# Kernel optimization log

Hardware: AMD Instinct MI355X
Metric: run time of the kernel (lower is better)

## Reference

```python
import jax, jax.numpy as jnp
import numpy as np

N = 8192
D_IN = 256
D_OUT = 256


def setup_inputs() -> dict:
    key = jax.random.key(0)
    k1, k2, k3 = jax.random.split(key, 3)
    input = jax.random.normal(k1, (N, D_IN), dtype=jnp.float32)
    adjacencyMatrix = jax.random.uniform(k2, (N, N), dtype=jnp.float32)
    W = jax.random.normal(k3, (D_OUT, D_IN), dtype=jnp.float32) * (1.0 / np.sqrt(D_IN))
    return {"input": input, "adjacencyMatrix": adjacencyMatrix, "W": W}


def reference(input, adjacencyMatrix, W):
    # degree^{-1/2} from row sums
    d_inv_sqrt = jnp.sum(adjacencyMatrix, axis=1) ** -0.5  # [N]
    # D^{-1/2} A D^{-1/2} as row/column scaling (same math as diag matmuls)
    A_norm = adjacencyMatrix * d_inv_sqrt[:, None] * d_inv_sqrt[None, :]  # [N, N]
    # A_norm @ X @ W^T (nn.Linear without bias)
    h = A_norm @ input            # [N, D_IN]
    return h @ W.T                # [N, D_OUT]
```

## Files before the change

### kernel.cpp

```cpp
#include <hip/hip_runtime.h>
#include <stdint.h>

#define NROWS 8192
#define KDIM  8192
#define DIN   256
#define DOUT  256

typedef __attribute__((ext_vector_type(8))) short bf16x8;
typedef __attribute__((ext_vector_type(4))) float f32x4;

__device__ __forceinline__ unsigned short f2bf(float f) {
    union { float f; unsigned u; } v; v.f = f;
    unsigned r = v.u + 0x7FFFu + ((v.u >> 16) & 1u);
    return (unsigned short)(r >> 16);
}

__device__ __forceinline__ void async_load16(const void* g, void* l) {
    __builtin_amdgcn_global_load_lds(
        (__attribute__((address_space(1))) void*)(void*)g,
        (__attribute__((address_space(3))) void*)l, 16, 0, 0);
}

__global__ __launch_bounds__(256) void k_rowsum(const float* __restrict__ A,
                                                float* __restrict__ dis) {
    const int wave = threadIdx.x >> 6, lane = threadIdx.x & 63;
    const int row = (blockIdx.x << 2) + wave;
    const float4* rp = (const float4*)(A + (size_t)row * KDIM);
    float s0 = 0.f, s1 = 0.f, s2 = 0.f, s3 = 0.f;
    #pragma unroll
    for (int it = 0; it < 32; it += 4) {
        float4 v0 = rp[(it + 0) * 64 + lane];
        float4 v1 = rp[(it + 1) * 64 + lane];
        float4 v2 = rp[(it + 2) * 64 + lane];
        float4 v3 = rp[(it + 3) * 64 + lane];
        s0 += (v0.x + v0.y) + (v0.z + v0.w);
        s1 += (v1.x + v1.y) + (v1.z + v1.w);
        s2 += (v2.x + v2.y) + (v2.z + v2.w);
        s3 += (v3.x + v3.y) + (v3.z + v3.w);
    }
    float s = (s0 + s1) + (s2 + s3);
    #pragma unroll
    for (int off = 32; off > 0; off >>= 1) s += __shfl_down(s, off, 64);
    if (lane == 0) dis[row] = rsqrtf(s);
}

__global__ __launch_bounds__(256, 2) void k_xw(const float* __restrict__ X,
                                               const float* __restrict__ W,
                                               const float* __restrict__ dis,
                                               unsigned short* __restrict__ Zst) {
    __shared__ short sX[64 * 72];
    __shared__ short sW[256 * 72];
    __shared__ float disS[64];
    const int tid = threadIdx.x;
    const int w = tid >> 6, lane = tid & 63, lm = lane & 15, lq = lane >> 4;
    const int j0 = blockIdx.x * 64;
    if (tid < 64) disS[tid] = dis[j0 + tid];
    f32x4 acc[4][4] = {};

    for (int s = 0; s < 4; ++s) {
        const int k0 = s * 64;
        #pragma unroll
        for (int i = 0; i < 4; ++i) {
            int e = tid + i * 256;
            int row = e >> 4, c4 = e & 15;
            float4 v = *(const float4*)(X + (size_t)(j0 + row) * DIN + k0 + c4 * 4);
            short4 b; b.x = (short)f2bf(v.x); b.y = (short)f2bf(v.y);
            b.z = (short)f2bf(v.z); b.w = (short)f2bf(v.w);
            *(short4*)&sX[row * 72 + c4 * 4] = b;
        }
        #pragma unroll
        for (int i = 0; i < 16; ++i) {
            int e = tid + i * 256;
            int row = e >> 4, c4 = e & 15;
            float4 v = *(const float4*)(W + (size_t)row * DIN + k0 + c4 * 4);
            short4 b; b.x = (short)f2bf(v.x); b.y = (short)f2bf(v.y);
            b.z = (short)f2bf(v.z); b.w = (short)f2bf(v.w);
            *(short4*)&sW[row * 72 + c4 * 4] = b;
        }
        __syncthreads();
        #pragma unroll
        for (int kk = 0; kk < 2; ++kk) {
            const int koff = kk * 32 + lq * 8;
            bf16x8 a[4], b[4];
            #pragma unroll
            for (int mt = 0; mt < 4; ++mt)
                a[mt] = *(const bf16x8*)&sX[(mt * 16 + lm) * 72 + koff];
            #pragma unroll
            for (int nt = 0; nt < 4; ++nt)
                b[nt] = *(const bf16x8*)&sW[(w * 64 + nt * 16 + lm) * 72 + koff];
            #pragma unroll
            for (int mt = 0; mt < 4; ++mt)
                #pragma unroll
                for (int nt = 0; nt < 4; ++nt)
                    acc[mt][nt] = __builtin_amdgcn_mfma_f32_16x16x32_bf16(
                        a[mt], b[nt], acc[mt][nt], 0, 0, 0);
        }
        __syncthreads();
    }

    #pragma unroll
    for (int mt = 0; mt < 4; ++mt)
        #pragma unroll
        for (int nt = 0; nt < 4; ++nt)
            #pragma unroll
            for (int r = 0; r < 4; ++r) {
                int jl = mt * 16 + lq * 4 + r;
                int n  = w * 64 + nt * 16 + lm;
                float v = acc[mt][nt][r] * disS[jl];
                sW[n * 72 + jl] = (short)f2bf(v);
            }
    __syncthreads();
    #pragma unroll
    for (int it = 0; it < 8; ++it) {
        int e = tid + it * 256;
        int n = e >> 3, ch = e & 7;
        bf16x8 val = *(const bf16x8*)&sW[n * 72 + ch * 8];
        *(bf16x8*)(Zst + (size_t)n * NROWS + j0 + ch * 8) = val;
    }
}

template <bool ATOMIC>
__global__ __launch_bounds__(512, 2) void k_gemm2(const float* __restrict__ A,
                                                  const unsigned short* __restrict__ Zst,
                                                  const float* __restrict__ dis,
                                                  float* __restrict__ out) {
    __shared__ short sA[2][128 * 72];
    __shared__ short sB[2][256 * 64];
    __shared__ float disS[128];
    const int tid = threadIdx.x;
    const int w = tid >> 6, lane = tid & 63, lm = lane & 15, lq = lane >> 4;
    const int wm = w >> 2, wn = w & 3;
    const int m0 = blockIdx.x * 128;
    const int split = blockIdx.y;
    const int kbase = split * 2048;
    if (tid < 128) disS[tid] = dis[m0 + tid];
    f32x4 acc[4][4] = {};
    const int swz_c = (lane & 7) ^ (lane >> 3);
    const int arow = tid >> 4, ac = tid & 15;
    float4 va[4];

#define LOAD_A(K0)                                                                   \
    do {                                                                             \
        _Pragma("unroll")                                                            \
        for (int i = 0; i < 4; ++i)                                                  \
            va[i] = *(const float4*)(A + (size_t)(m0 + arow + i * 32) * KDIM + (K0) + ac * 4); \
    } while (0)

#define WRITE_A(BUF)                                                                 \
    do {                                                                             \
        _Pragma("unroll")                                                            \
        for (int i = 0; i < 4; ++i) {                                                \
            short4 b; b.x = (short)f2bf(va[i].x); b.y = (short)f2bf(va[i].y);        \
            b.z = (short)f2bf(va[i].z); b.w = (short)f2bf(va[i].w);                  \
            *(short4*)&sA[BUF][(arow + i * 32) * 72 + ac * 4] = b;                   \
        }                                                                            \
    } while (0)

#define STAGE_B(BUF, K0)                                                             \
    do {                                                                             \
        const unsigned short* gB =                                                   \
            Zst + (size_t)(w * 32 + (lane >> 3)) * KDIM + (K0) + swz_c * 8;          \
        short* dst = &sB[BUF][w * 2048];                                             \
        _Pragma("unroll")                                                            \
        for (int i = 0; i < 4; ++i)                                                  \
            async_load16(gB + (size_t)i * 8 * KDIM, dst + i * 512);                  \
    } while (0)

#define COMPUTE(BUF)                                                                 \
    do {                                                                             \
        _Pragma("unroll")                                                            \
        for (int kk = 0; kk < 2; ++kk) {                                             \
            const int sc = (kk * 4 + lq) ^ (lm & 7);                                 \
            bf16x8 a[4], b[4];                                                       \
            _Pragma("unroll")                                                        \
            for (int mt = 0; mt < 4; ++mt)                                           \
                a[mt] = *(const bf16x8*)&sA[BUF][(wm * 64 + mt * 16 + lm) * 72 + kk * 32 + lq * 8]; \
            _Pragma("unroll")                                                        \
            for (int nt = 0; nt < 4; ++nt)                                           \
                b[nt] = *(const bf16x8*)&sB[BUF][(wn * 64 + nt * 16 + lm) * 64 + sc * 8]; \
            _Pragma("unroll")                                                        \
            for (int mt = 0; mt < 4; ++mt)                                           \
                _Pragma("unroll")                                                    \
                for (int nt = 0; nt < 4; ++nt)                                       \
                    acc[mt][nt] = __builtin_amdgcn_mfma_f32_16x16x32_bf16(           \
                        a[mt], b[nt], acc[mt][nt], 0, 0, 0);                         \
        }                                                                            \
    } while (0)

    LOAD_A(kbase);
    STAGE_B(0, kbase);
    WRITE_A(0);
    __syncthreads();

    int cur = 0;
    for (int s = 0; s < 31; ++s) {
        const int kn = kbase + (s + 1) * 64;
        LOAD_A(kn);
        STAGE_B(cur ^ 1, kn);
        COMPUTE(cur);
        WRITE_A(cur ^ 1);
        __syncthreads();
        cur ^= 1;
    }
    COMPUTE(cur);

#undef LOAD_A
#undef WRITE_A
#undef STAGE_B
#undef COMPUTE

    #pragma unroll
    for (int mt = 0; mt < 4; ++mt)
        #pragma unroll
        for (int nt = 0; nt < 4; ++nt) {
            int col = wn * 64 + nt * 16 + lm;
            #pragma unroll
            for (int r = 0; r < 4; ++r) {
                int rl = wm * 64 + mt * 16 + lq * 4 + r;
                float v = acc[mt][nt][r] * disS[rl];
                if (ATOMIC) {
                    atomicAdd(out + (size_t)(m0 + rl) * DOUT + col, v);
                } else {
                    out[(size_t)split * (NROWS * DOUT) + (size_t)(m0 + rl) * DOUT + col] = v;
                }
            }
        }
}

__global__ __launch_bounds__(256) void k_reduce(const float4* __restrict__ p,
                                                float4* __restrict__ out) {
    const size_t i = (size_t)blockIdx.x * 256 + threadIdx.x;
    const size_t stride = (size_t)NROWS * DOUT / 4;
    float4 a = p[i], b = p[i + stride], c = p[i + 2 * stride], d = p[i + 3 * stride];
    float4 r;
    r.x = (a.x + b.x) + (c.x + d.x);
    r.y = (a.y + b.y) + (c.y + d.y);
    r.z = (a.z + b.z) + (c.z + d.z);
    r.w = (a.w + b.w) + (c.w + d.w);
    out[i] = r;
}

extern "C" void kernel_launch(void* const* d_in, const int* in_sizes, int n_in,
                              void* d_out, int out_size, void* d_ws, size_t ws_size,
                              hipStream_t stream) {
    const float* X = (const float*)d_in[0];
    const float* A = (const float*)d_in[1];
    const float* W = (const float*)d_in[2];
    float* out = (float*)d_out;
    char* ws = (char*)d_ws;
    float* dis = (float*)ws;
    unsigned short* Zst = (unsigned short*)(ws + 32768);
    float* part = (float*)(ws + 32768 + 4194304);
    const size_t need = 32768 + 4194304 + 4ull * NROWS * DOUT * sizeof(float);

    k_rowsum<<<NROWS / 4, 256, 0, stream>>>(A, dis);
    k_xw<<<NROWS / 64, 256, 0, stream>>>(X, W, dis, Zst);
    if (ws_size >= need) {
        k_gemm2<false><<<dim3(NROWS / 128, 4), 512, 0, stream>>>(A, Zst, dis, part);
        k_reduce<<<(NROWS * DOUT / 4) / 256, 256, 0, stream>>>((const float4*)part,
                                                               (float4*)out);
    } else {
        hipMemsetAsync(d_out, 0, (size_t)out_size * sizeof(float), stream);
        k_gemm2<true><<<dim3(NROWS / 128, 4), 512, 0, stream>>>(A, Zst, dis, out);
    }
}
```

Baseline: 448.9 us.

## Merge rowsum and XW kernels; apply column degree scaling to A in GEMM

The row-sum kernel and the X·W^T kernel become one launch with disjoint block ranges, so the XW blocks no longer wait for degree computation. To allow this, the column scaling by d^{-1/2} moves out of the XW epilogue and into the big GEMM, where each A tile element is multiplied by dis[k] before bf16 conversion. This saves one kernel launch and lets the row sums overlap the small GEMM. The cost is an extra dis vector load and multiply per A tile in the main GEMM, and a change in bf16 rounding order.

```diff
diff --git a/kernel.cpp b/kernel.cpp
--- a/kernel.cpp
+++ b/kernel.cpp
@@ -21,40 +21,40 @@
         (__attribute__((address_space(3))) void*)l, 16, 0, 0);
 }
 
-__global__ __launch_bounds__(256) void k_rowsum(const float* __restrict__ A,
-                                                float* __restrict__ dis) {
-    const int wave = threadIdx.x >> 6, lane = threadIdx.x & 63;
-    const int row = (blockIdx.x << 2) + wave;
-    const float4* rp = (const float4*)(A + (size_t)row * KDIM);
-    float s0 = 0.f, s1 = 0.f, s2 = 0.f, s3 = 0.f;
-    #pragma unroll
-    for (int it = 0; it < 32; it += 4) {
-        float4 v0 = rp[(it + 0) * 64 + lane];
-        float4 v1 = rp[(it + 1) * 64 + lane];
-        float4 v2 = rp[(it + 2) * 64 + lane];
-        float4 v3 = rp[(it + 3) * 64 + lane];
-        s0 += (v0.x + v0.y) + (v0.z + v0.w);
-        s1 += (v1.x + v1.y) + (v1.z + v1.w);
-        s2 += (v2.x + v2.y) + (v2.z + v2.w);
-        s3 += (v3.x + v3.y) + (v3.z + v3.w);
-    }
-    float s = (s0 + s1) + (s2 + s3);
-    #pragma unroll
-    for (int off = 32; off > 0; off >>= 1) s += __shfl_down(s, off, 64);
-    if (lane == 0) dis[row] = rsqrtf(s);
-}
-
-__global__ __launch_bounds__(256, 2) void k_xw(const float* __restrict__ X,
-                                               const float* __restrict__ W,
-                                               const float* __restrict__ dis,
-                                               unsigned short* __restrict__ Zst) {
+__global__ __launch_bounds__(256) void k_pre(const float* __restrict__ A,
+                                             const float* __restrict__ X,
+                                             const float* __restrict__ W,
+                                             float* __restrict__ dis,
+                                             unsigned short* __restrict__ Yt) {
     __shared__ short sX[64 * 72];
     __shared__ short sW[256 * 72];
-    __shared__ float disS[64];
     const int tid = threadIdx.x;
+
+    if (blockIdx.x < 2048) {
+        const int wave = tid >> 6, lane = tid & 63;
+        const int row = (blockIdx.x << 2) + wave;
+        const float4* rp = (const float4*)(A + (size_t)row * KDIM);
+        float s0 = 0.f, s1 = 0.f, s2 = 0.f, s3 = 0.f;
+        #pragma unroll
+        for (int it = 0; it < 32; it += 4) {
+            float4 v0 = rp[(it + 0) * 64 + lane];
+            float4 v1 = rp[(it + 1) * 64 + lane];
+            float4 v2 = rp[(it + 2) * 64 + lane];
+            float4 v3 = rp[(it + 3) * 64 + lane];
+            s0 += (v0.x + v0.y) + (v0.z + v0.w);
+            s1 += (v1.x + v1.y) + (v1.z + v1.w);
+            s2 += (v2.x + v2.y) + (v2.z + v2.w);
+            s3 += (v3.x + v3.y) + (v3.z + v3.w);
+        }
+        float s = (s0 + s1) + (s2 + s3);
+        #pragma unroll
+        for (int off = 32; off > 0; off >>= 1) s += __shfl_down(s, off, 64);
+        if (lane == 0) dis[row] = rsqrtf(s);
+        return;
+    }
+
     const int w = tid >> 6, lane = tid & 63, lm = lane & 15, lq = lane >> 4;
-    const int j0 = blockIdx.x * 64;
-    if (tid < 64) disS[tid] = dis[j0 + tid];
+    const int j0 = (blockIdx.x - 2048) * 64;
     f32x4 acc[4][4] = {};
 
     for (int s = 0; s < 4; ++s) {
@@ -106,8 +106,7 @@
             for (int r = 0; r < 4; ++r) {
                 int jl = mt * 16 + lq * 4 + r;
                 int n  = w * 64 + nt * 16 + lm;
-                float v = acc[mt][nt][r] * disS[jl];
-                sW[n * 72 + jl] = (short)f2bf(v);
+                sW[n * 72 + jl] = (short)f2bf(acc[mt][nt][r]);
             }
     __syncthreads();
     #pragma unroll
@@ -115,7 +114,7 @@
         int e = tid + it * 256;
         int n = e >> 3, ch = e & 7;
         bf16x8 val = *(const bf16x8*)&sW[n * 72 + ch * 8];
-        *(bf16x8*)(Zst + (size_t)n * NROWS + j0 + ch * 8) = val;
+        *(bf16x8*)(Yt + (size_t)n * NROWS + j0 + ch * 8) = val;
     }
 }
 
@@ -138,9 +137,11 @@
     const int swz_c = (lane & 7) ^ (lane >> 3);
     const int arow = tid >> 4, ac = tid & 15;
     float4 va[4];
+    float4 vd;
 
 #define LOAD_A(K0)                                                                   \
     do {                                                                             \
+        vd = *(const float4*)(dis + (K0) + ac * 4);                                  \
         _Pragma("unroll")                                                            \
         for (int i = 0; i < 4; ++i)                                                  \
             va[i] = *(const float4*)(A + (size_t)(m0 + arow + i * 32) * KDIM + (K0) + ac * 4); \
@@ -150,8 +151,9 @@
     do {                                                                             \
         _Pragma("unroll")                                                            \
         for (int i = 0; i < 4; ++i) {                                                \
-            short4 b; b.x = (short)f2bf(va[i].x); b.y = (short)f2bf(va[i].y);        \
-            b.z = (short)f2bf(va[i].z); b.w = (short)f2bf(va[i].w);                  \
+            short4 b;                                                                \
+            b.x = (short)f2bf(va[i].x * vd.x); b.y = (short)f2bf(va[i].y * vd.y);    \
+            b.z = (short)f2bf(va[i].z * vd.z); b.w = (short)f2bf(va[i].w * vd.w);    \
             *(short4*)&sA[BUF][(arow + i * 32) * 72 + ac * 4] = b;                   \
         }                                                                            \
     } while (0)
@@ -249,18 +251,17 @@
     float* out = (float*)d_out;
     char* ws = (char*)d_ws;
     float* dis = (float*)ws;
-    unsigned short* Zst = (unsigned short*)(ws + 32768);
+    unsigned short* Yt = (unsigned short*)(ws + 32768);
     float* part = (float*)(ws + 32768 + 4194304);
     const size_t need = 32768 + 4194304 + 4ull * NROWS * DOUT * sizeof(float);
 
-    k_rowsum<<<NROWS / 4, 256, 0, stream>>>(A, dis);
-    k_xw<<<NROWS / 64, 256, 0, stream>>>(X, W, dis, Zst);
+    k_pre<<<2048 + NROWS / 64, 256, 0, stream>>>(A, X, W, dis, Yt);
     if (ws_size >= need) {
-        k_gemm2<false><<<dim3(NROWS / 128, 4), 512, 0, stream>>>(A, Zst, dis, part);
+        k_gemm2<false><<<dim3(NROWS / 128, 4), 512, 0, stream>>>(A, Yt, dis, part);
         k_reduce<<<(NROWS * DOUT / 4) / 256, 256, 0, stream>>>((const float4*)part,
                                                                (float4*)out);
     } else {
         hipMemsetAsync(d_out, 0, (size_t)out_size * sizeof(float), stream);
-        k_gemm2<true><<<dim3(NROWS / 128, 4), 512, 0, stream>>>(A, Zst, dis, out);
-    }
-}
+        k_gemm2<true><<<dim3(NROWS / 128, 4), 512, 0, stream>>>(A, Yt, dis, out);
+    }
+}
```

Result: slower. 463.4 us (+3.2%).

## Shrink big GEMM tile to 64 rows by 32-wide K with 256-thread blocks

Applied to the files above, without the earlier changes.

Rewrites the main A·Z GEMM to use 64-row M tiles, a 32-element K step, and 4 waves per block, each covering 64 output columns, in place of 128-row tiles with 8 waves. The grid doubles to 512 blocks, and launch bounds ask for 3 blocks per CU, aiming for more blocks in flight and better latency hiding across the 256 CUs. The trade-off is that each Z tile is now reloaded for only 64 rows of A, so Z traffic doubles. The B tile also loses its XOR swizzle, which may cause LDS bank conflicts.

```diff
diff --git a/kernel.cpp b/kernel.cpp
--- a/kernel.cpp
+++ b/kernel.cpp
@@ -120,71 +120,66 @@
 }
 
 template <bool ATOMIC>
-__global__ __launch_bounds__(512, 2) void k_gemm2(const float* __restrict__ A,
+__global__ __launch_bounds__(256, 3) void k_gemm5(const float* __restrict__ A,
                                                   const unsigned short* __restrict__ Zst,
                                                   const float* __restrict__ dis,
                                                   float* __restrict__ out) {
-    __shared__ short sA[2][128 * 72];
-    __shared__ short sB[2][256 * 64];
-    __shared__ float disS[128];
+    __shared__ short sA[2][64 * 40];
+    __shared__ short sB[2][256 * 32];
+    __shared__ float disS[64];
     const int tid = threadIdx.x;
     const int w = tid >> 6, lane = tid & 63, lm = lane & 15, lq = lane >> 4;
-    const int wm = w >> 2, wn = w & 3;
-    const int m0 = blockIdx.x * 128;
+    const int m0 = blockIdx.x * 64;
     const int split = blockIdx.y;
     const int kbase = split * 2048;
-    if (tid < 128) disS[tid] = dis[m0 + tid];
+    if (tid < 64) disS[tid] = dis[m0 + tid];
     f32x4 acc[4][4] = {};
-    const int swz_c = (lane & 7) ^ (lane >> 3);
-    const int arow = tid >> 4, ac = tid & 15;
-    float4 va[4];
+    const int arow = tid >> 2, acol = (tid & 3) * 8;
+    float4 va[2];
 
 #define LOAD_A(K0)                                                                   \
     do {                                                                             \
+        const float* ap = A + (size_t)(m0 + arow) * KDIM + (K0) + acol;              \
+        va[0] = *(const float4*)ap;                                                  \
+        va[1] = *(const float4*)(ap + 4);                                            \
+    } while (0)
+
+#define WRITE_A(BUF)                                                                 \
+    do {                                                                             \
+        short4 b0, b1;                                                               \
+        b0.x = (short)f2bf(va[0].x); b0.y = (short)f2bf(va[0].y);                    \
+        b0.z = (short)f2bf(va[0].z); b0.w = (short)f2bf(va[0].w);                    \
+        b1.x = (short)f2bf(va[1].x); b1.y = (short)f2bf(va[1].y);                    \
+        b1.z = (short)f2bf(va[1].z); b1.w = (short)f2bf(va[1].w);                    \
+        *(short4*)&sA[BUF][arow * 40 + acol] = b0;                                   \
+        *(short4*)&sA[BUF][arow * 40 + acol + 4] = b1;                               \
+    } while (0)
+
+#define STAGE_B(BUF, K0)                                                             \
+    do {                                                                             \
+        const unsigned short* gB =                                                   \
+            Zst + (size_t)(w * 64 + (lane >> 2)) * KDIM + (K0) + (lane & 3) * 8;     \
+        short* dst = &sB[BUF][w * 2048];                                             \
         _Pragma("unroll")                                                            \
         for (int i = 0; i < 4; ++i)                                                  \
-            va[i] = *(const float4*)(A + (size_t)(m0 + arow + i * 32) * KDIM + (K0) + ac * 4); \
-    } while (0)
-
-#define WRITE_A(BUF)                                                                 \
-    do {                                                                             \
-        _Pragma("unroll")                                                            \
-        for (int i = 0; i < 4; ++i) {                                                \
-            short4 b; b.x = (short)f2bf(va[i].x); b.y = (short)f2bf(va[i].y);        \
-            b.z = (short)f2bf(va[i].z); b.w = (short)f2bf(va[i].w);                  \
-            *(short4*)&sA[BUF][(arow + i * 32) * 72 + ac * 4] = b;                   \
-        }                                                                            \
-    } while (0)
-
-#define STAGE_B(BUF, K0)                                                             \
-    do {                                                                             \
-        const unsigned short* gB =                                                   \
-            Zst + (size_t)(w * 32 + (lane >> 3)) * KDIM + (K0) + swz_c * 8;          \
-        short* dst = &sB[BUF][w * 2048];                                             \
-        _Pragma("unroll")                                                            \
-        for (int i = 0; i < 4; ++i)                                                  \
-            async_load16(gB + (size_t)i * 8 * KDIM, dst + i * 512);                  \
+            async_load16(gB + (size_t)i * 16 * KDIM, dst + i * 512);                 \
     } while (0)
 
 #define COMPUTE(BUF)                                                                 \
     do {                                                                             \
-        _Pragma("unroll")                                                            \
-        for (int kk = 0; kk < 2; ++kk) {                                             \
-            const int sc = (kk * 4 + lq) ^ (lm & 7);                                 \
-            bf16x8 a[4], b[4];                                                       \
-            _Pragma("unroll")                                                        \
-            for (int mt = 0; mt < 4; ++mt)                                           \
-                a[mt] = *(const bf16x8*)&sA[BUF][(wm * 64 + mt * 16 + lm) * 72 + kk * 32 + lq * 8]; \
+        bf16x8 a[4], b[4];                                                           \
+        _Pragma("unroll")                                                            \
+        for (int mt = 0; mt < 4; ++mt)                                               \
+            a[mt] = *(const bf16x8*)&sA[BUF][(mt * 16 + lm) * 40 + lq * 8];          \
+        _Pragma("unroll")                                                            \
+        for (int nt = 0; nt < 4; ++nt)                                               \
+            b[nt] = *(const bf16x8*)&sB[BUF][(w * 64 + nt * 16 + lm) * 32 + lq * 8]; \
+        _Pragma("unroll")                                                            \
+        for (int mt = 0; mt < 4; ++mt)                                               \
             _Pragma("unroll")                                                        \
             for (int nt = 0; nt < 4; ++nt)                                           \
-                b[nt] = *(const bf16x8*)&sB[BUF][(wn * 64 + nt * 16 + lm) * 64 + sc * 8]; \
-            _Pragma("unroll")                                                        \
-            for (int mt = 0; mt < 4; ++mt)                                           \
-                _Pragma("unroll")                                                    \
-                for (int nt = 0; nt < 4; ++nt)                                       \
-                    acc[mt][nt] = __builtin_amdgcn_mfma_f32_16x16x32_bf16(           \
-                        a[mt], b[nt], acc[mt][nt], 0, 0, 0);                         \
-        }                                                                            \
+                acc[mt][nt] = __builtin_amdgcn_mfma_f32_16x16x32_bf16(               \
+                    a[mt], b[nt], acc[mt][nt], 0, 0, 0);                             \
     } while (0)
 
     LOAD_A(kbase);
@@ -193,8 +188,8 @@
     __syncthreads();
 
     int cur = 0;
-    for (int s = 0; s < 31; ++s) {
-        const int kn = kbase + (s + 1) * 64;
+    for (int s = 0; s < 63; ++s) {
+        const int kn = kbase + (s + 1) * 32;
         LOAD_A(kn);
         STAGE_B(cur ^ 1, kn);
         COMPUTE(cur);
@@ -213,10 +208,10 @@
     for (int mt = 0; mt < 4; ++mt)
         #pragma unroll
         for (int nt = 0; nt < 4; ++nt) {
-            int col = wn * 64 + nt * 16 + lm;
+            int col = w * 64 + nt * 16 + lm;
             #pragma unroll
             for (int r = 0; r < 4; ++r) {
-                int rl = wm * 64 + mt * 16 + lq * 4 + r;
+                int rl = mt * 16 + lq * 4 + r;
                 float v = acc[mt][nt][r] * disS[rl];
                 if (ATOMIC) {
                     atomicAdd(out + (size_t)(m0 + rl) * DOUT + col, v);
@@ -256,11 +251,11 @@
     k_rowsum<<<NROWS / 4, 256, 0, stream>>>(A, dis);
     k_xw<<<NROWS / 64, 256, 0, stream>>>(X, W, dis, Zst);
     if (ws_size >= need) {
-        k_gemm2<false><<<dim3(NROWS / 128, 4), 512, 0, stream>>>(A, Zst, dis, part);
+        k_gemm5<false><<<dim3(NROWS / 64, 4), 256, 0, stream>>>(A, Zst, dis, part);
         k_reduce<<<(NROWS * DOUT / 4) / 256, 256, 0, stream>>>((const float4*)part,
                                                                (float4*)out);
     } else {
         hipMemsetAsync(d_out, 0, (size_t)out_size * sizeof(float), stream);
-        k_gemm2<true><<<dim3(NROWS / 128, 4), 512, 0, stream>>>(A, Zst, dis, out);
-    }
-}
+        k_gemm5<true><<<dim3(NROWS / 64, 4), 256, 0, stream>>>(A, Zst, dis, out);
+    }
+}
```

Result: slower. 490.2 us (+9.2%).

## Emit bf16 copy of A in rowsum and run register-only MFMA GEMM on it

Applied to the files above, without the earlier changes.

The row-sum pass now also writes a bf16 copy of the adjacency matrix to workspace. A new GEMM kernel then reads that bf16 copy together with Zst directly from global memory into registers, double-buffered, with no LDS staging, instead of re-reading fp32 A and converting it. This halves the bytes read by the main GEMM but adds a 128 MB bf16 write and needs extra workspace. Fragments are loaded uncoalesced straight from global memory, and the path is only taken if the workspace is large enough.

```diff
diff --git a/kernel.cpp b/kernel.cpp
--- a/kernel.cpp
+++ b/kernel.cpp
@@ -21,11 +21,14 @@
         (__attribute__((address_space(3))) void*)l, 16, 0, 0);
 }
 
+template <bool STORE>
 __global__ __launch_bounds__(256) void k_rowsum(const float* __restrict__ A,
-                                                float* __restrict__ dis) {
+                                                float* __restrict__ dis,
+                                                unsigned short* __restrict__ Abf) {
     const int wave = threadIdx.x >> 6, lane = threadIdx.x & 63;
     const int row = (blockIdx.x << 2) + wave;
     const float4* rp = (const float4*)(A + (size_t)row * KDIM);
+    unsigned short* op = STORE ? (Abf + (size_t)row * KDIM) : nullptr;
     float s0 = 0.f, s1 = 0.f, s2 = 0.f, s3 = 0.f;
     #pragma unroll
     for (int it = 0; it < 32; it += 4) {
@@ -33,6 +36,21 @@
         float4 v1 = rp[(it + 1) * 64 + lane];
         float4 v2 = rp[(it + 2) * 64 + lane];
         float4 v3 = rp[(it + 3) * 64 + lane];
+        if (STORE) {
+            short4 b0, b1, b2, b3;
+            b0.x = (short)f2bf(v0.x); b0.y = (short)f2bf(v0.y);
+            b0.z = (short)f2bf(v0.z); b0.w = (short)f2bf(v0.w);
+            b1.x = (short)f2bf(v1.x); b1.y = (short)f2bf(v1.y);
+            b1.z = (short)f2bf(v1.z); b1.w = (short)f2bf(v1.w);
+            b2.x = (short)f2bf(v2.x); b2.y = (short)f2bf(v2.y);
+            b2.z = (short)f2bf(v2.z); b2.w = (short)f2bf(v2.w);
+            b3.x = (short)f2bf(v3.x); b3.y = (short)f2bf(v3.y);
+            b3.z = (short)f2bf(v3.z); b3.w = (short)f2bf(v3.w);
+            *(short4*)(op + ((size_t)(it + 0) * 64 + lane) * 4) = b0;
+            *(short4*)(op + ((size_t)(it + 1) * 64 + lane) * 4) = b1;
+            *(short4*)(op + ((size_t)(it + 2) * 64 + lane) * 4) = b2;
+            *(short4*)(op + ((size_t)(it + 3) * 64 + lane) * 4) = b3;
+        }
         s0 += (v0.x + v0.y) + (v0.z + v0.w);
         s1 += (v1.x + v1.y) + (v1.z + v1.w);
         s2 += (v2.x + v2.y) + (v2.z + v2.w);
@@ -117,6 +135,85 @@
         bf16x8 val = *(const bf16x8*)&sW[n * 72 + ch * 8];
         *(bf16x8*)(Zst + (size_t)n * NROWS + j0 + ch * 8) = val;
     }
+}
+
+template <bool ATOMIC>
+__global__ __launch_bounds__(256, 2) void k_gemm_reg(const unsigned short* __restrict__ Abf,
+                                                     const unsigned short* __restrict__ Zst,
+                                                     const float* __restrict__ dis,
+                                                     float* __restrict__ out) {
+    const int tid = threadIdx.x;
+    const int w = tid >> 6, lane = tid & 63, lm = lane & 15, lq = lane >> 4;
+    const int m0 = blockIdx.x * 64;
+    const int split = blockIdx.y;
+    const int kbase = split * 2048;
+    f32x4 acc[4][4] = {};
+    const unsigned short* aBase = Abf + (size_t)(m0 + lm) * KDIM + lq * 8;
+    const unsigned short* bBase = Zst + (size_t)(w * 64 + lm) * KDIM + lq * 8;
+    bf16x8 a0[8], a1[8], b0[8], b1[8];
+
+#define LOADF(AA, BB, K0)                                                                 \
+    do {                                                                                  \
+        _Pragma("unroll")                                                                 \
+        for (int mt = 0; mt < 4; ++mt) {                                                  \
+            AA[mt * 2 + 0] = *(const bf16x8*)(aBase + (size_t)(mt * 16) * KDIM + (K0));   \
+            AA[mt * 2 + 1] = *(const bf16x8*)(aBase + (size_t)(mt * 16) * KDIM + (K0) + 32); \
+        }                                                                                 \
+        _Pragma("unroll")                                                                 \
+        for (int nt = 0; nt < 4; ++nt) {                                                  \
+            BB[nt * 2 + 0] = *(const bf16x8*)(bBase + (size_t)(nt * 16) * KDIM + (K0));   \
+            BB[nt * 2 + 1] = *(const bf16x8*)(bBase + (size_t)(nt * 16) * KDIM + (K0) + 32); \
+        }                                                                                 \
+    } while (0)
+
+#define COMPUTE(AA, BB)                                                                   \
+    do {                                                                                  \
+        _Pragma("unroll")                                                                 \
+        for (int kk = 0; kk < 2; ++kk)                                                    \
+            _Pragma("unroll")                                                             \
+            for (int mt = 0; mt < 4; ++mt)                                                \
+                _Pragma("unroll")                                                         \
+                for (int nt = 0; nt < 4; ++nt)                                            \
+                    acc[mt][nt] = __builtin_amdgcn_mfma_f32_16x16x32_bf16(                \
+                        AA[mt * 2 + kk], BB[nt * 2 + kk], acc[mt][nt], 0, 0, 0);          \
+    } while (0)
+
+    LOADF(a0, b0, kbase);
+    for (int s = 0; s < 30; s += 2) {
+        LOADF(a1, b1, kbase + (s + 1) * 64);
+        COMPUTE(a0, b0);
+        LOADF(a0, b0, kbase + (s + 2) * 64);
+        COMPUTE(a1, b1);
+    }
+    LOADF(a1, b1, kbase + 31 * 64);
+    COMPUTE(a0, b0);
+    COMPUTE(a1, b1);
+
+#undef LOADF
+#undef COMPUTE
+
+    float dm[16];
+    #pragma unroll
+    for (int mt = 0; mt < 4; ++mt)
+        #pragma unroll
+        for (int r = 0; r < 4; ++r)
+            dm[mt * 4 + r] = dis[m0 + mt * 16 + lq * 4 + r];
+    #pragma unroll
+    for (int mt = 0; mt < 4; ++mt)
+        #pragma unroll
+        for (int nt = 0; nt < 4; ++nt) {
+            int col = w * 64 + nt * 16 + lm;
+            #pragma unroll
+            for (int r = 0; r < 4; ++r) {
+                int rl = mt * 16 + lq * 4 + r;
+                float v = acc[mt][nt][r] * dm[mt * 4 + r];
+                if (ATOMIC) {
+                    atomicAdd(out + (size_t)(m0 + rl) * DOUT + col, v);
+                } else {
+                    out[(size_t)split * (NROWS * DOUT) + (size_t)(m0 + rl) * DOUT + col] = v;
+                }
+            }
+        }
 }
 
 template <bool ATOMIC>
@@ -251,15 +348,25 @@
     float* dis = (float*)ws;
     unsigned short* Zst = (unsigned short*)(ws + 32768);
     float* part = (float*)(ws + 32768 + 4194304);
-    const size_t need = 32768 + 4194304 + 4ull * NROWS * DOUT * sizeof(float);
-
-    k_rowsum<<<NROWS / 4, 256, 0, stream>>>(A, dis);
-    k_xw<<<NROWS / 64, 256, 0, stream>>>(X, W, dis, Zst);
-    if (ws_size >= need) {
+    unsigned short* Abf = (unsigned short*)(ws + 32768 + 4194304 + 33554432);
+    const size_t need_mid  = 32768 + 4194304 + 4ull * NROWS * DOUT * sizeof(float);
+    const size_t need_full = need_mid + (size_t)NROWS * KDIM * sizeof(unsigned short);
+
+    if (ws_size >= need_full) {
+        k_rowsum<true><<<NROWS / 4, 256, 0, stream>>>(A, dis, Abf);
+        k_xw<<<NROWS / 64, 256, 0, stream>>>(X, W, dis, Zst);
+        k_gemm_reg<false><<<dim3(NROWS / 64, 4), 256, 0, stream>>>(Abf, Zst, dis, part);
+        k_reduce<<<(NROWS * DOUT / 4) / 256, 256, 0, stream>>>((const float4*)part,
+                                                               (float4*)out);
+    } else if (ws_size >= need_mid) {
+        k_rowsum<false><<<NROWS / 4, 256, 0, stream>>>(A, dis, nullptr);
+        k_xw<<<NROWS / 64, 256, 0, stream>>>(X, W, dis, Zst);
         k_gemm2<false><<<dim3(NROWS / 128, 4), 512, 0, stream>>>(A, Zst, dis, part);
         k_reduce<<<(NROWS * DOUT / 4) / 256, 256, 0, stream>>>((const float4*)part,
                                                                (float4*)out);
     } else {
+        k_rowsum<false><<<NROWS / 4, 256, 0, stream>>>(A, dis, nullptr);
+        k_xw<<<NROWS / 64, 256, 0, stream>>>(X, W, dis, Zst);
         hipMemsetAsync(d_out, 0, (size_t)out_size * sizeof(float), stream);
         k_gemm2<true><<<dim3(NROWS / 128, 4), 512, 0, stream>>>(A, Zst, dis, out);
     }
```

After: 524.7 us. 1.17x slower.
